# Kernel optimization log

Hardware: AMD Instinct MI355X
Metric: run time of the kernel (lower is better)

The kernel has to match this reference:

```python
import jax, jax.numpy as jnp
import numpy as np

BN_EPS = 1e-5

def setup_inputs() -> dict:
    key = jax.random.key(0)
    ks = jax.random.split(key, 5)
    B, C, H, W = 4, 64, 64, 64
    s = 1.0 / np.sqrt(C)
    return {
        "x": jax.random.normal(ks[0], (B, C, H, W), dtype=jnp.float32),
        "Wk": jax.random.normal(ks[1], (C, C), dtype=jnp.float32) * s,
        "Wq": jax.random.normal(ks[2], (C, C), dtype=jnp.float32) * s,
        "Wv": jax.random.normal(ks[3], (C, C), dtype=jnp.float32) * s,
        "W2": jax.random.normal(ks[4], (C, C), dtype=jnp.float32) * s,
        "gamma": jnp.ones((C,), dtype=jnp.float32),
        "beta": jnp.zeros((C,), dtype=jnp.float32),
        "running_mean": jnp.zeros((C,), dtype=jnp.float32),
        "running_var": jnp.ones((C,), dtype=jnp.float32),
    }

def reference(x, Wk, Wq, Wv, W2, gamma, beta, running_mean, running_var):
    B, C, H, W = x.shape
    N = H * W
    xf = x.reshape(B, C, N)                      # flatten spatial -> (B,C,N)
    # 1x1 convs (no bias) == channel matmuls
    k = jnp.einsum('oc,bcn->bon', Wk, xf)        # (B,C,N)
    q = jnp.einsum('oc,bcn->bon', Wq, xf)
    v = jnp.einsum('oc,bcn->bon', Wv, xf)
    # scores[b,n,m] = sum_c k[b,c,n] * q[b,c,m]  (note: no 1/sqrt(d) scaling, as in source)
    scores = jnp.einsum('bcn,bcm->bnm', k, q)    # (B,N,N)
    p = jax.nn.softmax(scores, axis=2)
    # att[b,c,n] = sum_m p[b,n,m] * v[b,c,m]
    att = jnp.einsum('bnm,bcm->bcn', p, v)       # (B,C,N)
    y = jnp.einsum('oc,bcn->bon', W2, att)       # 1x1 conv
    inv = gamma / jnp.sqrt(running_var + BN_EPS)
    y = y * inv[None, :, None] + (beta - running_mean * inv)[None, :, None]
    y = jax.nn.relu(y)
    return y.reshape(B, C, H, W) + x
```

## Files before the change

### kernel.cpp

```cpp
#include <hip/hip_runtime.h>
#include <math.h>

#define CH   64
#define NTOT 4096
#define NB   4

typedef short  short4v  __attribute__((ext_vector_type(4)));
typedef short  short8v  __attribute__((ext_vector_type(8)));
typedef float  floatx4  __attribute__((ext_vector_type(4)));

static __device__ __forceinline__ short f2bf(float f) {
    union { float f; unsigned int u; } v; v.f = f;
    unsigned int r = v.u + 0x7FFFu + ((v.u >> 16) & 1u);
    return (short)(r >> 16);
}

__global__ __launch_bounds__(256) void qkv_proj(
    const float* __restrict__ x,
    const float* __restrict__ Wk, const float* __restrict__ Wq,
    const float* __restrict__ Wv,
    short* __restrict__ kT, short* __restrict__ qT, short* __restrict__ vg)
{
    __shared__ __align__(16) float xs [64][68];
    __shared__ __align__(16) float wkT[64][68];
    __shared__ __align__(16) float wqT[64][68];
    __shared__ __align__(16) float wvT[64][68];

    const int tid = threadIdx.x;
    const int b  = blockIdx.x >> 6;
    const int n0 = (blockIdx.x & 63) * 64;
    const float* xb = x + (size_t)b * CH * NTOT;

    for (int i = tid; i < 64 * 64; i += 256) {
        int c = i >> 6, n = i & 63;
        xs[c][n] = xb[(size_t)c * NTOT + n0 + n];
    }
    for (int i = tid; i < 64 * 64; i += 256) {
        int o = i >> 6, c = i & 63;
        wkT[c][o] = Wk[i];
        wqT[c][o] = Wq[i];
        wvT[c][o] = Wv[i];
    }
    __syncthreads();

    const int to = tid >> 4, tn = tid & 15;
    const int ob = to * 4, nb = tn * 4;
    float ak[4][4] = {}, aq[4][4] = {}, av[4][4] = {};

    for (int c = 0; c < 64; ++c) {
        float4 xv = *(const float4*)&xs [c][nb];
        float4 k4 = *(const float4*)&wkT[c][ob];
        float4 q4 = *(const float4*)&wqT[c][ob];
        float4 v4 = *(const float4*)&wvT[c][ob];
        float xa[4] = {xv.x, xv.y, xv.z, xv.w};
        float ka[4] = {k4.x, k4.y, k4.z, k4.w};
        float qa[4] = {q4.x, q4.y, q4.z, q4.w};
        float va[4] = {v4.x, v4.y, v4.z, v4.w};
        #pragma unroll
        for (int i = 0; i < 4; ++i)
            #pragma unroll
            for (int j = 0; j < 4; ++j) {
                ak[i][j] += ka[i] * xa[j];
                aq[i][j] += qa[i] * xa[j];
                av[i][j] += va[i] * xa[j];
            }
    }

    #pragma unroll
    for (int j = 0; j < 4; ++j) {
        size_t row = (size_t)(b << 12) + n0 + nb + j;
        short4v kk = { f2bf(ak[0][j]), f2bf(ak[1][j]), f2bf(ak[2][j]), f2bf(ak[3][j]) };
        short4v qq = { f2bf(aq[0][j]), f2bf(aq[1][j]), f2bf(aq[2][j]), f2bf(aq[3][j]) };
        *(short4v*)&kT[row * 64 + ob] = kk;
        *(short4v*)&qT[row * 64 + ob] = qq;
    }
    #pragma unroll
    for (int i = 0; i < 4; ++i) {
        short4v vv = { f2bf(av[i][0]), f2bf(av[i][1]), f2bf(av[i][2]), f2bf(av[i][3]) };
        *(short4v*)&vg[(((size_t)(b << 6) + ob + i) << 12) + n0 + nb] = vv;
    }
}

__global__ __launch_bounds__(256) void attn_partial(
    const short* __restrict__ kT, const short* __restrict__ qT,
    const short* __restrict__ vg,
    float* __restrict__ opart, float* __restrict__ mlpart)
{
    __shared__ __align__(16) short smem[18432];

    const int tid = threadIdx.x;
    const int w  = tid >> 6;
    const int l  = tid & 63;
    const int g  = l >> 4;
    const int ln = l & 15;

    const int bid  = blockIdx.x;
    const int xcd  = bid & 7, grp = bid >> 3;
    const int bk   = (xcd << 1) | (grp >> 6);
    const int b    = bk >> 2;
    const int kc   = bk & 3;
    const int qblk = grp & 63;
    const int n0   = qblk << 6;
    const int part = (b << 8) | (kc << 6) | qblk;
    const int kbase = kc << 10;

    const short* kTb = kT + ((size_t)(b << 12) + n0) * 64;
    const short* qTb = qT + ((size_t)b << 12) * 64;
    const short* vb  = vg + ((size_t)(b << 6) << 12);

    short* const kTs = smem;
    short* const qS  = smem + 4608;
    short* const vS  = smem + 9216;
    short* const PsW = smem + 13824 + w * 1152;

    {
        int r0 = tid >> 3, c8 = (tid & 7) << 3;
        *(short8v*)&kTs[r0 * 72 + c8]        = *(const short8v*)&kTb[r0 * 64 + c8];
        *(short8v*)&kTs[(r0 + 32) * 72 + c8] = *(const short8v*)&kTb[(r0 + 32) * 64 + c8];
    }
    __syncthreads();

    short8v bS0 = *(const short8v*)&kTs[((w << 4) + ln) * 72 + (g << 3)];
    short8v bS1 = *(const short8v*)&kTs[((w << 4) + ln) * 72 + 32 + (g << 3)];

    float mrun = -1e30f;
    float lrun = 0.f;
    floatx4 acc_o[4];
    #pragma unroll
    for (int ct = 0; ct < 4; ++ct) acc_o[ct] = (floatx4){0.f, 0.f, 0.f, 0.f};

    const int i0 = tid, i1 = tid + 256;

    short8v pf[4];
    pf[0] = *(const short8v*)&qTb[(size_t)(kbase + (i0 >> 3)) * 64 + ((i0 & 7) << 3)];
    pf[1] = *(const short8v*)&qTb[(size_t)(kbase + (i1 >> 3)) * 64 + ((i1 & 7) << 3)];
    pf[2] = *(const short8v*)&vb[(size_t)(i0 >> 3) * 4096 + kbase + ((i0 & 7) << 3)];
    pf[3] = *(const short8v*)&vb[(size_t)(i1 >> 3) * 4096 + kbase + ((i1 & 7) << 3)];

    for (int t = 0; t < 16; ++t) {
        __syncthreads();
        *(short8v*)&qS[(i0 >> 3) * 72 + ((i0 & 7) << 3)] = pf[0];
        *(short8v*)&qS[(i1 >> 3) * 72 + ((i1 & 7) << 3)] = pf[1];
        *(short8v*)&vS[(i0 >> 3) * 72 + ((i0 & 7) << 3)] = pf[2];
        *(short8v*)&vS[(i1 >> 3) * 72 + ((i1 & 7) << 3)] = pf[3];
        __syncthreads();
        if (t < 15) {
            int m1 = kbase + ((t + 1) << 6);
            pf[0] = *(const short8v*)&qTb[(size_t)(m1 + (i0 >> 3)) * 64 + ((i0 & 7) << 3)];
            pf[1] = *(const short8v*)&qTb[(size_t)(m1 + (i1 >> 3)) * 64 + ((i1 & 7) << 3)];
            pf[2] = *(const short8v*)&vb[(size_t)(i0 >> 3) * 4096 + m1 + ((i0 & 7) << 3)];
            pf[3] = *(const short8v*)&vb[(size_t)(i1 >> 3) * 4096 + m1 + ((i1 & 7) << 3)];
        }

        floatx4 sacc[4];
        #pragma unroll
        for (int mt = 0; mt < 4; ++mt) {
            short8v a0 = *(const short8v*)&qS[((mt << 4) + ln) * 72 + (g << 3)];
            short8v a1 = *(const short8v*)&qS[((mt << 4) + ln) * 72 + 32 + (g << 3)];
            floatx4 acc = (floatx4){0.f, 0.f, 0.f, 0.f};
            acc = __builtin_amdgcn_mfma_f32_16x16x32_bf16(a0, bS0, acc, 0, 0, 0);
            acc = __builtin_amdgcn_mfma_f32_16x16x32_bf16(a1, bS1, acc, 0, 0, 0);
            sacc[mt] = acc;
        }

        float mx = sacc[0][0];
        #pragma unroll
        for (int mt = 0; mt < 4; ++mt)
            #pragma unroll
            for (int r = 0; r < 4; ++r) mx = fmaxf(mx, sacc[mt][r]);
        mx = fmaxf(mx, __shfl_xor(mx, 16));
        mx = fmaxf(mx, __shfl_xor(mx, 32));

        float mnew = fmaxf(mrun, mx);
        float fs = __expf(mrun - mnew);
        mrun = mnew;

        float s = 0.f;
        #pragma unroll
        for (int mt = 0; mt < 4; ++mt) {
            float p0 = __expf(sacc[mt][0] - mnew);
            float p1 = __expf(sacc[mt][1] - mnew);
            float p2 = __expf(sacc[mt][2] - mnew);
            float p3 = __expf(sacc[mt][3] - mnew);
            s += (p0 + p1) + (p2 + p3);
            short4v p4 = { f2bf(p0), f2bf(p1), f2bf(p2), f2bf(p3) };
            *(short4v*)&PsW[ln * 72 + (mt << 4) + (g << 2)] = p4;
        }
        s += __shfl_xor(s, 16);
        s += __shfl_xor(s, 32);
        lrun = lrun * fs + s;

        #pragma unroll
        for (int ct = 0; ct < 4; ++ct) {
            acc_o[ct][0] *= fs; acc_o[ct][1] *= fs;
            acc_o[ct][2] *= fs; acc_o[ct][3] *= fs;
        }

        short8v bp0 = *(const short8v*)&PsW[ln * 72 + (g << 3)];
        short8v bp1 = *(const short8v*)&PsW[ln * 72 + 32 + (g << 3)];
        #pragma unroll
        for (int ct = 0; ct < 4; ++ct) {
            short8v a0 = *(const short8v*)&vS[((ct << 4) + ln) * 72 + (g << 3)];
            short8v a1 = *(const short8v*)&vS[((ct << 4) + ln) * 72 + 32 + (g << 3)];
            acc_o[ct] = __builtin_amdgcn_mfma_f32_16x16x32_bf16(a0, bp0, acc_o[ct], 0, 0, 0);
            acc_o[ct] = __builtin_amdgcn_mfma_f32_16x16x32_bf16(a1, bp1, acc_o[ct], 0, 0, 0);
        }
    }

    __syncthreads();
    float* xp = (float*)(smem + 4608);
    #pragma unroll
    for (int ct = 0; ct < 4; ++ct)
        #pragma unroll
        for (int r = 0; r < 4; ++r)
            xp[((w << 4) + ln) * 68 + (ct << 4) + (g << 2) + r] = acc_o[ct][r];
    if (g == 0) {
        mlpart[(size_t)part * 128 + (w << 4) + ln]      = mrun;
        mlpart[(size_t)part * 128 + 64 + (w << 4) + ln] = lrun;
    }
    __syncthreads();
    {
        int q = tid >> 2, c16 = (tid & 3) << 4;
        float* Ob = opart + (size_t)part * 4096 + q * 64 + c16;
        #pragma unroll
        for (int i = 0; i < 4; ++i)
            *(float4*)&Ob[i << 2] = *(const float4*)&xp[q * 68 + c16 + (i << 2)];
    }
}

__global__ __launch_bounds__(256) void attn_merge(
    const float* __restrict__ opart, const float* __restrict__ mlpart,
    const float* __restrict__ W2,
    const float* __restrict__ gamma, const float* __restrict__ beta,
    const float* __restrict__ rmean, const float* __restrict__ rvar,
    const float* __restrict__ x, float* __restrict__ out)
{
    __shared__ __align__(16) short attL[64 * 72];
    __shared__ __align__(16) short w2s [64 * 72];
    __shared__ float wgt[4][64];
    __shared__ float linv[64];

    const int tid = threadIdx.x;
    const int w  = tid >> 6;
    const int l  = tid & 63;
    const int g  = l >> 4;
    const int ln = l & 15;

    const int b    = blockIdx.x >> 6;
    const int qblk = blockIdx.x & 63;
    const int n0   = qblk << 6;
    const int part0 = (b << 8) | qblk;

    if (tid < 64) {
        float m0 = mlpart[(size_t)(part0)        * 128 + tid];
        float m1 = mlpart[(size_t)(part0 + 64)   * 128 + tid];
        float m2 = mlpart[(size_t)(part0 + 128)  * 128 + tid];
        float m3 = mlpart[(size_t)(part0 + 192)  * 128 + tid];
        float l0 = mlpart[(size_t)(part0)        * 128 + 64 + tid];
        float l1 = mlpart[(size_t)(part0 + 64)   * 128 + 64 + tid];
        float l2 = mlpart[(size_t)(part0 + 128)  * 128 + 64 + tid];
        float l3 = mlpart[(size_t)(part0 + 192)  * 128 + 64 + tid];
        float mm = fmaxf(fmaxf(m0, m1), fmaxf(m2, m3));
        float w0 = __expf(m0 - mm), w1 = __expf(m1 - mm);
        float w2 = __expf(m2 - mm), w3 = __expf(m3 - mm);
        wgt[0][tid] = w0; wgt[1][tid] = w1; wgt[2][tid] = w2; wgt[3][tid] = w3;
        linv[tid] = 1.0f / (w0 * l0 + w1 * l1 + w2 * l2 + w3 * l3);
    }
    for (int i = tid; i < 1024; i += 256) {
        int r = i >> 4, c4 = (i & 15) << 2;
        float4 wv = *(const float4*)&W2[(r << 6) + c4];
        short4v s4 = { f2bf(wv.x), f2bf(wv.y), f2bf(wv.z), f2bf(wv.w) };
        *(short4v*)&w2s[r * 72 + c4] = s4;
    }
    __syncthreads();

    {
        int q = tid >> 2, c16 = (tid & 3) << 4;
        float a[16] = {};
        #pragma unroll
        for (int kc = 0; kc < 4; ++kc) {
            float wk = wgt[kc][q];
            const float* Ob = opart + (size_t)(part0 + (kc << 6)) * 4096 + q * 64 + c16;
            #pragma unroll
            for (int i = 0; i < 4; ++i) {
                float4 o4 = *(const float4*)&Ob[i << 2];
                a[(i << 2) + 0] += wk * o4.x;
                a[(i << 2) + 1] += wk * o4.y;
                a[(i << 2) + 2] += wk * o4.z;
                a[(i << 2) + 3] += wk * o4.w;
            }
        }
        float li = linv[q];
        #pragma unroll
        for (int i = 0; i < 4; ++i) {
            short4v s4 = { f2bf(a[(i << 2) + 0] * li), f2bf(a[(i << 2) + 1] * li),
                           f2bf(a[(i << 2) + 2] * li), f2bf(a[(i << 2) + 3] * li) };
            *(short4v*)&attL[q * 72 + c16 + (i << 2)] = s4;
        }
    }
    __syncthreads();

    short8v bA0 = *(const short8v*)&attL[((w << 4) + ln) * 72 + (g << 3)];
    short8v bA1 = *(const short8v*)&attL[((w << 4) + ln) * 72 + 32 + (g << 3)];
    const int nq = n0 + (w << 4) + ln;
    #pragma unroll
    for (int ot = 0; ot < 4; ++ot) {
        short8v a0 = *(const short8v*)&w2s[((ot << 4) + ln) * 72 + (g << 3)];
        short8v a1 = *(const short8v*)&w2s[((ot << 4) + ln) * 72 + 32 + (g << 3)];
        floatx4 acc = (floatx4){0.f, 0.f, 0.f, 0.f};
        acc = __builtin_amdgcn_mfma_f32_16x16x32_bf16(a0, bA0, acc, 0, 0, 0);
        acc = __builtin_amdgcn_mfma_f32_16x16x32_bf16(a1, bA1, acc, 0, 0, 0);
        int o0 = (ot << 4) + (g << 2);
        float4 gm = *(const float4*)&gamma[o0];
        float4 bt = *(const float4*)&beta [o0];
        float4 rm = *(const float4*)&rmean[o0];
        float4 rv = *(const float4*)&rvar [o0];
        float gma[4] = {gm.x, gm.y, gm.z, gm.w};
        float bta[4] = {bt.x, bt.y, bt.z, bt.w};
        float rma[4] = {rm.x, rm.y, rm.z, rm.w};
        float rva[4] = {rv.x, rv.y, rv.z, rv.w};
        #pragma unroll
        for (int r = 0; r < 4; ++r) {
            float inv  = gma[r] * rsqrtf(rva[r] + 1e-5f);
            float bias = bta[r] - rma[r] * inv;
            size_t ga = (((size_t)(b << 6) + o0 + r) << 12) + nq;
            out[ga] = fmaxf(acc[r] * inv + bias, 0.f) + x[ga];
        }
    }
}

extern "C" void kernel_launch(void* const* d_in, const int* in_sizes, int n_in,
                              void* d_out, int out_size, void* d_ws, size_t ws_size,
                              hipStream_t stream)
{
    const float* x     = (const float*)d_in[0];
    const float* Wk    = (const float*)d_in[1];
    const float* Wq    = (const float*)d_in[2];
    const float* Wv    = (const float*)d_in[3];
    const float* W2    = (const float*)d_in[4];
    const float* gamma = (const float*)d_in[5];
    const float* beta  = (const float*)d_in[6];
    const float* rmean = (const float*)d_in[7];
    const float* rvar  = (const float*)d_in[8];
    float* out = (float*)d_out;

    const size_t plane = (size_t)NB * NTOT * CH;
    short* kT = (short*)d_ws;
    short* qT = kT + plane;
    short* vv = qT + plane;
    float* opart  = (float*)(vv + plane);
    float* mlpart = opart + (size_t)1024 * 4096;

    qkv_proj    <<<dim3(256),  dim3(256), 0, stream>>>(x, Wk, Wq, Wv, kT, qT, vv);
    attn_partial<<<dim3(1024), dim3(256), 0, stream>>>(kT, qT, vv, opart, mlpart);
    attn_merge  <<<dim3(256),  dim3(256), 0, stream>>>(opart, mlpart, W2, gamma, beta,
                                                       rmean, rvar, x, out);
}
```

Before: 67.58 us.

## Use packed bf16 conversion, exp2 softmax with lazy rescale, and finer QKV grid

Replaces the software bf16 rounding with the hardware v_cvt_pk_bf16_f32 packed conversion throughout. The online softmax now uses exp2 with a pre-scaled max and skips the accumulator rescale when no lane's running max increases. The QKV projection kernel is split into 512 blocks of 32 columns for more parallelism, with vectorized x loads. Together these aim to cut VALU work in the attention inner loop and to improve occupancy in the projection, at the cost of a wave-uniform branch and slightly different rounding behaviour.

New measurement: 69.28 us. 1.03x slower.

```diff
diff --git a/kernel.cpp b/kernel.cpp
--- a/kernel.cpp
+++ b/kernel.cpp
@@ -1,18 +1,22 @@
 #include <hip/hip_runtime.h>
-#include <math.h>
 
 #define CH   64
 #define NTOT 4096
 #define NB   4
+#define L2E  1.44269504088896340736f
 
 typedef short  short4v  __attribute__((ext_vector_type(4)));
 typedef short  short8v  __attribute__((ext_vector_type(8)));
 typedef float  floatx4  __attribute__((ext_vector_type(4)));
 
-static __device__ __forceinline__ short f2bf(float f) {
-    union { float f; unsigned int u; } v; v.f = f;
-    unsigned int r = v.u + 0x7FFFu + ((v.u >> 16) & 1u);
-    return (short)(r >> 16);
+static __device__ __forceinline__ unsigned pk2bf(float lo, float hi) {
+    unsigned r;
+    asm("v_cvt_pk_bf16_f32 %0, %1, %2" : "=v"(r) : "v"(lo), "v"(hi));
+    return r;
+}
+
+static __device__ __forceinline__ float ex2(float x) {
+    return __builtin_amdgcn_exp2f(x);
 }
 
 __global__ __launch_bounds__(256) void qkv_proj(
@@ -21,19 +25,20 @@
     const float* __restrict__ Wv,
     short* __restrict__ kT, short* __restrict__ qT, short* __restrict__ vg)
 {
-    __shared__ __align__(16) float xs [64][68];
+    __shared__ __align__(16) float xs [64][36];
     __shared__ __align__(16) float wkT[64][68];
     __shared__ __align__(16) float wqT[64][68];
     __shared__ __align__(16) float wvT[64][68];
 
     const int tid = threadIdx.x;
-    const int b  = blockIdx.x >> 6;
-    const int n0 = (blockIdx.x & 63) * 64;
+    const int b  = blockIdx.x >> 7;
+    const int n0 = (blockIdx.x & 127) * 32;
     const float* xb = x + (size_t)b * CH * NTOT;
 
-    for (int i = tid; i < 64 * 64; i += 256) {
-        int c = i >> 6, n = i & 63;
-        xs[c][n] = xb[(size_t)c * NTOT + n0 + n];
+    {
+        int c = tid >> 2, nn = (tid & 3) << 3;
+        *(float4*)&xs[c][nn]     = *(const float4*)&xb[(size_t)c * NTOT + n0 + nn];
+        *(float4*)&xs[c][nn + 4] = *(const float4*)&xb[(size_t)c * NTOT + n0 + nn + 4];
     }
     for (int i = tid; i < 64 * 64; i += 256) {
         int o = i >> 6, c = i & 63;
@@ -44,41 +49,40 @@
     __syncthreads();
 
     const int to = tid >> 4, tn = tid & 15;
-    const int ob = to * 4, nb = tn * 4;
-    float ak[4][4] = {}, aq[4][4] = {}, av[4][4] = {};
+    const int ob = to * 4, nb = tn * 2;
+    float ak[4][2] = {}, aq[4][2] = {}, av[4][2] = {};
 
     for (int c = 0; c < 64; ++c) {
-        float4 xv = *(const float4*)&xs [c][nb];
+        float x0 = xs[c][nb], x1 = xs[c][nb + 1];
         float4 k4 = *(const float4*)&wkT[c][ob];
         float4 q4 = *(const float4*)&wqT[c][ob];
         float4 v4 = *(const float4*)&wvT[c][ob];
-        float xa[4] = {xv.x, xv.y, xv.z, xv.w};
         float ka[4] = {k4.x, k4.y, k4.z, k4.w};
         float qa[4] = {q4.x, q4.y, q4.z, q4.w};
         float va[4] = {v4.x, v4.y, v4.z, v4.w};
         #pragma unroll
-        for (int i = 0; i < 4; ++i)
-            #pragma unroll
-            for (int j = 0; j < 4; ++j) {
-                ak[i][j] += ka[i] * xa[j];
-                aq[i][j] += qa[i] * xa[j];
-                av[i][j] += va[i] * xa[j];
-            }
-    }
-
-    #pragma unroll
-    for (int j = 0; j < 4; ++j) {
+        for (int i = 0; i < 4; ++i) {
+            ak[i][0] += ka[i] * x0;  ak[i][1] += ka[i] * x1;
+            aq[i][0] += qa[i] * x0;  aq[i][1] += qa[i] * x1;
+            av[i][0] += va[i] * x0;  av[i][1] += va[i] * x1;
+        }
+    }
+
+    #pragma unroll
+    for (int j = 0; j < 2; ++j) {
         size_t row = (size_t)(b << 12) + n0 + nb + j;
-        short4v kk = { f2bf(ak[0][j]), f2bf(ak[1][j]), f2bf(ak[2][j]), f2bf(ak[3][j]) };
-        short4v qq = { f2bf(aq[0][j]), f2bf(aq[1][j]), f2bf(aq[2][j]), f2bf(aq[3][j]) };
-        *(short4v*)&kT[row * 64 + ob] = kk;
-        *(short4v*)&qT[row * 64 + ob] = qq;
-    }
-    #pragma unroll
-    for (int i = 0; i < 4; ++i) {
-        short4v vv = { f2bf(av[i][0]), f2bf(av[i][1]), f2bf(av[i][2]), f2bf(av[i][3]) };
-        *(short4v*)&vg[(((size_t)(b << 6) + ob + i) << 12) + n0 + nb] = vv;
-    }
+        uint2 kk, qq;
+        kk.x = pk2bf(ak[0][j], ak[1][j]);
+        kk.y = pk2bf(ak[2][j], ak[3][j]);
+        qq.x = pk2bf(aq[0][j], aq[1][j]);
+        qq.y = pk2bf(aq[2][j], aq[3][j]);
+        *(uint2*)&kT[row * 64 + ob] = kk;
+        *(uint2*)&qT[row * 64 + ob] = qq;
+    }
+    #pragma unroll
+    for (int i = 0; i < 4; ++i)
+        *(unsigned*)&vg[(((size_t)(b << 6) + ob + i) << 12) + n0 + nb] =
+            pk2bf(av[i][0], av[i][1]);
 }
 
 __global__ __launch_bounds__(256) void attn_partial(
@@ -100,8 +104,8 @@
     const int b    = bk >> 2;
     const int kc   = bk & 3;
     const int qblk = grp & 63;
+    const int part = (b << 8) | (kc << 6) | qblk;
     const int n0   = qblk << 6;
-    const int part = (b << 8) | (kc << 6) | qblk;
     const int kbase = kc << 10;
 
     const short* kTb = kT + ((size_t)(b << 12) + n0) * 64;
@@ -171,30 +175,35 @@
         mx = fmaxf(mx, __shfl_xor(mx, 16));
         mx = fmaxf(mx, __shfl_xor(mx, 32));
 
-        float mnew = fmaxf(mrun, mx);
-        float fs = __expf(mrun - mnew);
-        mrun = mnew;
-
+        if (!__all(mx <= mrun)) {
+            float mnew = fmaxf(mrun, mx);
+            float fs = ex2((mrun - mnew) * L2E);
+            mrun = mnew;
+            lrun *= fs;
+            #pragma unroll
+            for (int ct = 0; ct < 4; ++ct) {
+                acc_o[ct][0] *= fs; acc_o[ct][1] *= fs;
+                acc_o[ct][2] *= fs; acc_o[ct][3] *= fs;
+            }
+        }
+
+        const float nm = -mrun * L2E;
         float s = 0.f;
         #pragma unroll
         for (int mt = 0; mt < 4; ++mt) {
-            float p0 = __expf(sacc[mt][0] - mnew);
-            float p1 = __expf(sacc[mt][1] - mnew);
-            float p2 = __expf(sacc[mt][2] - mnew);
-            float p3 = __expf(sacc[mt][3] - mnew);
+            float p0 = ex2(__builtin_fmaf(sacc[mt][0], L2E, nm));
+            float p1 = ex2(__builtin_fmaf(sacc[mt][1], L2E, nm));
+            float p2 = ex2(__builtin_fmaf(sacc[mt][2], L2E, nm));
+            float p3 = ex2(__builtin_fmaf(sacc[mt][3], L2E, nm));
             s += (p0 + p1) + (p2 + p3);
-            short4v p4 = { f2bf(p0), f2bf(p1), f2bf(p2), f2bf(p3) };
-            *(short4v*)&PsW[ln * 72 + (mt << 4) + (g << 2)] = p4;
+            uint2 pkv;
+            pkv.x = pk2bf(p0, p1);
+            pkv.y = pk2bf(p2, p3);
+            *(uint2*)&PsW[ln * 72 + (mt << 4) + (g << 2)] = pkv;
         }
         s += __shfl_xor(s, 16);
         s += __shfl_xor(s, 32);
-        lrun = lrun * fs + s;
-
-        #pragma unroll
-        for (int ct = 0; ct < 4; ++ct) {
-            acc_o[ct][0] *= fs; acc_o[ct][1] *= fs;
-            acc_o[ct][2] *= fs; acc_o[ct][3] *= fs;
-        }
+        lrun += s;
 
         short8v bp0 = *(const short8v*)&PsW[ln * 72 + (g << 3)];
         short8v bp1 = *(const short8v*)&PsW[ln * 72 + 32 + (g << 3)];
@@ -261,16 +270,18 @@
         float l2 = mlpart[(size_t)(part0 + 128)  * 128 + 64 + tid];
         float l3 = mlpart[(size_t)(part0 + 192)  * 128 + 64 + tid];
         float mm = fmaxf(fmaxf(m0, m1), fmaxf(m2, m3));
-        float w0 = __expf(m0 - mm), w1 = __expf(m1 - mm);
-        float w2 = __expf(m2 - mm), w3 = __expf(m3 - mm);
+        float w0 = ex2((m0 - mm) * L2E), w1 = ex2((m1 - mm) * L2E);
+        float w2 = ex2((m2 - mm) * L2E), w3 = ex2((m3 - mm) * L2E);
         wgt[0][tid] = w0; wgt[1][tid] = w1; wgt[2][tid] = w2; wgt[3][tid] = w3;
         linv[tid] = 1.0f / (w0 * l0 + w1 * l1 + w2 * l2 + w3 * l3);
     }
     for (int i = tid; i < 1024; i += 256) {
         int r = i >> 4, c4 = (i & 15) << 2;
         float4 wv = *(const float4*)&W2[(r << 6) + c4];
-        short4v s4 = { f2bf(wv.x), f2bf(wv.y), f2bf(wv.z), f2bf(wv.w) };
-        *(short4v*)&w2s[r * 72 + c4] = s4;
+        uint2 s4;
+        s4.x = pk2bf(wv.x, wv.y);
+        s4.y = pk2bf(wv.z, wv.w);
+        *(uint2*)&w2s[r * 72 + c4] = s4;
     }
     __syncthreads();
 
@@ -293,9 +304,10 @@
         float li = linv[q];
         #pragma unroll
         for (int i = 0; i < 4; ++i) {
-            short4v s4 = { f2bf(a[(i << 2) + 0] * li), f2bf(a[(i << 2) + 1] * li),
-                           f2bf(a[(i << 2) + 2] * li), f2bf(a[(i << 2) + 3] * li) };
-            *(short4v*)&attL[q * 72 + c16 + (i << 2)] = s4;
+            uint2 s4;
+            s4.x = pk2bf(a[(i << 2) + 0] * li, a[(i << 2) + 1] * li);
+            s4.y = pk2bf(a[(i << 2) + 2] * li, a[(i << 2) + 3] * li);
+            *(uint2*)&attL[q * 72 + c16 + (i << 2)] = s4;
         }
     }
     __syncthreads();
@@ -321,7 +333,7 @@
         float rva[4] = {rv.x, rv.y, rv.z, rv.w};
         #pragma unroll
         for (int r = 0; r < 4; ++r) {
-            float inv  = gma[r] * rsqrtf(rva[r] + 1e-5f);
+            float inv  = gma[r] * __frsqrt_rn(rva[r] + 1e-5f);
             float bias = bta[r] - rma[r] * inv;
             size_t ga = (((size_t)(b << 6) + o0 + r) << 12) + nq;
             out[ga] = fmaxf(acc[r] * inv + bias, 0.f) + x[ga];
@@ -351,7 +363,7 @@
     float* opart  = (float*)(vv + plane);
     float* mlpart = opart + (size_t)1024 * 4096;
 
-    qkv_proj    <<<dim3(256),  dim3(256), 0, stream>>>(x, Wk, Wq, Wv, kT, qT, vv);
+    qkv_proj    <<<dim3(512),  dim3(256), 0, stream>>>(x, Wk, Wq, Wv, kT, qT, vv);
     attn_partial<<<dim3(1024), dim3(256), 0, stream>>>(kT, qT, vv, opart, mlpart);
     attn_merge  <<<dim3(256),  dim3(256), 0, stream>>>(opart, mlpart, W2, gamma, beta,
                                                        rmean, rvar, x, out);
```
